# Optimization experiments

Measured on AMD Instinct MI355X. Metric: run time of the kernel, lower is better.

Reference implementation:

```python
import jax, jax.numpy as jnp
import numpy as np

SECURE_MIN = 1e-5
EPS = 1e-20
N_ITER = 10

def _l1_normalize(t, axis):
    # F.normalize(p=1): t / max(||t||_1, eps); t is nonnegative here so |t| = t
    n = jnp.sum(jnp.abs(t), axis=axis, keepdims=True)
    return t / jnp.maximum(n, EPS)

def setup_inputs() -> dict:
    key = jax.random.key(0)
    kx, kw = jax.random.split(key)
    B, F_in, F_out = 2048, 4096, 2048
    x = jax.random.uniform(kx, (B, F_in), dtype=jnp.float32)
    W = jax.random.uniform(kw, (F_out, F_in), dtype=jnp.float32)
    return {"x": x, "W": W}

def reference(x, W):
    B = x.shape[0]
    F_out = W.shape[0]
    # normalize_weights: clamp to secure min, L1-normalize each row (over input dim)
    Wn = _l1_normalize(jnp.clip(W, SECURE_MIN), axis=1)  # (F_out, F_in)
    # _prepare_input: L1 normalize over feature dim
    xn = _l1_normalize(x, axis=-1)  # (B, F_in)
    # _reset_h: uniform h over output units
    h0 = jnp.full((B, F_out), 1.0 / F_out, dtype=x.dtype)

    def step(h, _):
        # _reconstruct: h @ W -> input space
        recon = h @ Wn                                   # (B, F_in)
        recon = jnp.clip(recon, SECURE_MIN)              # _secure_tensor
        recon = _l1_normalize(recon, axis=-1)            # normalize_reconstruction
        update = (xn / recon) @ Wn.T                     # _forward, (B, F_out)
        h = h * update                                   # multiplicative NNMF update
        h = _l1_normalize(jnp.clip(h, SECURE_MIN), axis=-1)  # _process_h
        return h, None

    h, _ = jax.lax.scan(step, h0, None, length=N_ITER)
    return h
```

## Files before the change

### kernel.cpp

```cpp
#include <hip/hip_runtime.h>
#include <stdint.h>
#include <stddef.h>

#define B_DIM 2048
#define FIN   4096
#define FOUT  2048
#define NITER 10
#define SMIN  1e-5f

#define WSCALE 16384.0f
#define HSCALE 256.0f
#define OUTSCALE1 (1.0f / 4194304.0f)
#define RS_I8 56.0f

typedef float floatx16 __attribute__((ext_vector_type(16)));
typedef int   intx4    __attribute__((ext_vector_type(4)));
typedef int   intx8    __attribute__((ext_vector_type(8)));
typedef int   intx16   __attribute__((ext_vector_type(16)));

__device__ inline unsigned short f2bf(float f) {
    unsigned int u = __float_as_uint(f);
    u += 0x7fffu + ((u >> 16) & 1u);
    return (unsigned short)(u >> 16);
}
__device__ inline float bflo(unsigned int u) { return __uint_as_float(u << 16); }
__device__ inline float bfhi(unsigned int u) { return __uint_as_float(u & 0xffff0000u); }
__device__ inline unsigned int pack2(float a, float b) {
    return (unsigned int)f2bf(a) | ((unsigned int)f2bf(b) << 16);
}
__device__ inline unsigned short f2h(float f) {
    union { _Float16 h; unsigned short u; } c;
    c.h = (_Float16)f;
    return c.u;
}
__device__ inline float h2f(unsigned short u) {
    union { _Float16 h; unsigned short u; } c;
    c.u = u;
    return (float)c.h;
}

__device__ inline void async16(const void* g, void* l) {
    __builtin_amdgcn_global_load_lds(
        (const __attribute__((address_space(1))) void*)g,
        (__attribute__((address_space(3))) void*)l, 16, 0, 0);
}

__device__ inline float block_row_sum(float v) {
    #pragma unroll
    for (int o = 32; o > 0; o >>= 1) v += __shfl_down(v, o, 64);
    __shared__ float red[4];
    const int lane = threadIdx.x & 63, w = threadIdx.x >> 6;
    if (lane == 0) red[w] = v;
    __syncthreads();
    return red[0] + red[1] + red[2] + red[3];
}

__device__ inline void block_sum_max(float s, float m, float* os, float* om) {
    #pragma unroll
    for (int o = 32; o > 0; o >>= 1) {
        s += __shfl_down(s, o, 64);
        m = fmaxf(m, __shfl_down(m, o, 64));
    }
    __shared__ float rs[4], rm[4];
    const int lane = threadIdx.x & 63, w = threadIdx.x >> 6;
    if (lane == 0) { rs[w] = s; rm[w] = m; }
    __syncthreads();
    *os = (rs[0] + rs[1]) + (rs[2] + rs[3]);
    *om = fmaxf(fmaxf(rm[0], rm[1]), fmaxf(rm[2], rm[3]));
}

__global__ __launch_bounds__(256) void k_norm_w(const float* __restrict__ W,
                                                unsigned char* __restrict__ Wn8,
                                                unsigned char* __restrict__ WnI8,
                                                float* __restrict__ dq) {
    const int row = blockIdx.x;
    const float4* src = (const float4*)(W + (size_t)row * FIN);
    float4 vals[4];
    float s = 0.f, m = 0.f;
    #pragma unroll
    for (int i = 0; i < 4; ++i) {
        float4 v = src[i * 256 + threadIdx.x];
        v.x = fmaxf(v.x, SMIN); v.y = fmaxf(v.y, SMIN);
        v.z = fmaxf(v.z, SMIN); v.w = fmaxf(v.w, SMIN);
        vals[i] = v;
        s += (v.x + v.y) + (v.z + v.w);
        m = fmaxf(m, fmaxf(fmaxf(v.x, v.y), fmaxf(v.z, v.w)));
    }
    block_sum_max(s, m, &s, &m);
    s = fmaxf(s, 1e-20f);
    const float inv8 = WSCALE / s;
    const float qi = 126.f / m;
    if (threadIdx.x == 0) dq[row] = m / (126.f * RS_I8 * s);
    unsigned int* d8 = (unsigned int*)(Wn8 + (size_t)row * FIN);
    unsigned int* di = (unsigned int*)(WnI8 + (size_t)row * FIN);
    #pragma unroll
    for (int i = 0; i < 4; ++i) {
        float4 v = vals[i];
        unsigned int u = 0;
        u = (unsigned int)__builtin_amdgcn_cvt_pk_fp8_f32(v.x * inv8, v.y * inv8, (int)u, false);
        u = (unsigned int)__builtin_amdgcn_cvt_pk_fp8_f32(v.z * inv8, v.w * inv8, (int)u, true);
        d8[i * 256 + threadIdx.x] = u;
        const int b0 = (int)(v.x * qi + 0.5f);
        const int b1 = (int)(v.y * qi + 0.5f);
        const int b2 = (int)(v.z * qi + 0.5f);
        const int b3 = (int)(v.w * qi + 0.5f);
        di[i * 256 + threadIdx.x] =
            (unsigned int)b0 | ((unsigned int)b1 << 8) |
            ((unsigned int)b2 << 16) | ((unsigned int)b3 << 24);
    }
}

__global__ __launch_bounds__(256) void k_norm_x(const float* __restrict__ x,
                                                unsigned int* __restrict__ xnb) {
    const int row = blockIdx.x;
    const float4* src = (const float4*)(x + (size_t)row * FIN);
    float4 vals[4];
    float s = 0.f;
    #pragma unroll
    for (int j = 0; j < 2; ++j) {
        const int idx = j * 256 + threadIdx.x;
        float4 a = src[2 * idx], b = src[2 * idx + 1];
        vals[2 * j] = a; vals[2 * j + 1] = b;
        s += (fabsf(a.x) + fabsf(a.y)) + (fabsf(a.z) + fabsf(a.w));
        s += (fabsf(b.x) + fabsf(b.y)) + (fabsf(b.z) + fabsf(b.w));
    }
    s = block_row_sum(s);
    const float inv = 1.f / fmaxf(s, 1e-20f);
    uint4* dst = (uint4*)(xnb + (size_t)row * (FIN / 2));
    #pragma unroll
    for (int j = 0; j < 2; ++j) {
        float4 a = vals[2 * j], b = vals[2 * j + 1];
        uint4 o;
        o.x = pack2(a.x * inv, a.y * inv);
        o.y = pack2(a.z * inv, a.w * inv);
        o.z = pack2(b.x * inv, b.y * inv);
        o.w = pack2(b.z * inv, b.w * inv);
        dst[j * 256 + threadIdx.x] = o;
    }
}

__global__ __launch_bounds__(256) void k_transpose_fp8(const unsigned char* __restrict__ src,
                                                       unsigned char* __restrict__ dst) {
    __shared__ unsigned char tile[32][33];
    const int bi = blockIdx.x * 32, bo = blockIdx.y * 32;
    const int tx = threadIdx.x, ty = threadIdx.y;
    #pragma unroll
    for (int j = 0; j < 4; ++j)
        tile[ty + j * 8][tx] = src[(size_t)(bo + ty + j * 8) * FIN + bi + tx];
    __syncthreads();
    #pragma unroll
    for (int j = 0; j < 4; ++j)
        dst[(size_t)(bi + ty + j * 8) * FOUT + bo + tx] = tile[tx][ty + j * 8];
}

__global__ __launch_bounds__(256) void k_init_h(unsigned int* __restrict__ h16,
                                                unsigned int* __restrict__ h8u) {
    const int i = blockIdx.x * blockDim.x + threadIdx.x;
    uint2 v; v.x = 0x10001000u; v.y = 0x10001000u;
    ((uint2*)h16)[i] = v;
    h8u[i] = 0x20202020u;
}

__global__ __launch_bounds__(256) void k_gemm_fp8(const unsigned char* __restrict__ A,
                                                  const unsigned char* __restrict__ Bm,
                                                  unsigned short* __restrict__ C,
                                                  int N, int K) {
    __shared__ __align__(16) unsigned char As[2][128 * 128];
    __shared__ __align__(16) unsigned char Bs[2][128 * 128];
    const int tid  = threadIdx.x;
    const int wave = tid >> 6;
    const int lane = tid & 63;

    const int id = blockIdx.y * 32 + blockIdx.x;
    const int j8 = id & 7, s = id >> 3;
    const int bm = ((j8 >> 2) * 8 + (s >> 3)) * 128;
    const int bn = ((j8 & 3) * 8 + (s & 7)) * 128;

    const int wr = (wave >> 1) * 64;
    const int wc = (wave & 1) * 64;
    const int l31 = lane & 31;
    const int half = lane >> 5;

    floatx16 acc[2][2] = {};

    const int lr = lane >> 3;
    const int ks = ((lane & 7) ^ lr) * 16;
    const unsigned char* ga = A  + (size_t)(bm + wave * 32 + lr) * K + ks;
    const unsigned char* gb = Bm + (size_t)(bn + wave * 32 + lr) * K + ks;

    auto stage = [&](int k0, int buf) {
        #pragma unroll
        for (int j = 0; j < 4; ++j) {
            async16(ga + (size_t)j * 8 * K + k0, &As[buf][wave * 4096 + j * 1024]);
            async16(gb + (size_t)j * 8 * K + k0, &Bs[buf][wave * 4096 + j * 1024]);
        }
    };

    const int nt = K >> 7;
    stage(0, 0);
    int cur = 0;
    for (int t = 0; t < nt; ++t) {
        __syncthreads();
        if (t + 1 < nt) stage((t + 1) << 7, cur ^ 1);

        const int sw = l31 & 7;
        #pragma unroll
        for (int m = 0; m < 2; ++m) {
            const int c0 = ((4 * m + 2 * half) ^ sw) << 4;
            const int c1 = ((4 * m + 2 * half + 1) ^ sw) << 4;
            intx8 af[2], bf[2];
            #pragma unroll
            for (int tt = 0; tt < 2; ++tt) {
                const int ra = (wr + tt * 32 + l31) * 128;
                const int rb = (wc + tt * 32 + l31) * 128;
                intx4 a0 = *(const intx4*)&As[cur][ra + c0];
                intx4 a1 = *(const intx4*)&As[cur][ra + c1];
                intx4 b0 = *(const intx4*)&Bs[cur][rb + c0];
                intx4 b1 = *(const intx4*)&Bs[cur][rb + c1];
                af[tt] = (intx8){a0.x, a0.y, a0.z, a0.w, a1.x, a1.y, a1.z, a1.w};
                bf[tt] = (intx8){b0.x, b0.y, b0.z, b0.w, b1.x, b1.y, b1.z, b1.w};
            }
            #pragma unroll
            for (int mt = 0; mt < 2; ++mt)
                #pragma unroll
                for (int nt2 = 0; nt2 < 2; ++nt2)
                    acc[mt][nt2] = __builtin_amdgcn_mfma_scale_f32_32x32x64_f8f6f4(
                        af[mt], bf[nt2], acc[mt][nt2],
                        0, 0, 0, 0x7F7F7F7Fu, 0, 0x7F7F7F7Fu);
        }
        cur ^= 1;
    }

    const int row0 = 4 * half;
    #pragma unroll
    for (int mt = 0; mt < 2; ++mt) {
        #pragma unroll
        for (int nt2 = 0; nt2 < 2; ++nt2) {
            #pragma unroll
            for (int reg = 0; reg < 16; ++reg) {
                const int rr = bm + wr + mt * 32 + row0 + (reg & 3) + 8 * (reg >> 2);
                const int cc = bn + wc + nt2 * 32 + l31;
                C[(size_t)rr * N + cc] = f2bf(acc[mt][nt2][reg] * OUTSCALE1);
            }
        }
    }
}

__global__ __launch_bounds__(256) void k_gemm_i8(const unsigned char* __restrict__ A,
                                                 const unsigned char* __restrict__ Bm,
                                                 const float* __restrict__ dq,
                                                 unsigned short* __restrict__ C,
                                                 int N, int K, int Ksub) {
    __shared__ __align__(16) unsigned char As[2][128 * 128];
    __shared__ __align__(16) unsigned char Bs[2][128 * 128];
    const int tid  = threadIdx.x;
    const int wave = tid >> 6;
    const int lane = tid & 63;

    const int id = blockIdx.y * 16 + blockIdx.x;
    const int j8 = id & 7, s = id >> 3;
    const int bm = ((j8 >> 1) * 4 + (s >> 3)) * 128;
    const int bn = ((j8 & 1) * 8 + (s & 7)) * 128;

    const int kz = blockIdx.z * Ksub;
    const int wr = (wave >> 1) * 64;
    const int wc = (wave & 1) * 64;
    const int l31 = lane & 31;
    const int half = lane >> 5;

    intx16 acc[2][2] = {};

    const int lr = lane >> 3;
    const int ks = ((lane & 7) ^ lr) * 16;
    const unsigned char* ga = A  + (size_t)(bm + wave * 32 + lr) * K + ks;
    const unsigned char* gb = Bm + (size_t)(bn + wave * 32 + lr) * K + ks;

    auto stage = [&](int k0, int buf) {
        #pragma unroll
        for (int j = 0; j < 4; ++j) {
            async16(ga + (size_t)j * 8 * K + k0, &As[buf][wave * 4096 + j * 1024]);
            async16(gb + (size_t)j * 8 * K + k0, &Bs[buf][wave * 4096 + j * 1024]);
        }
    };

    const int nt = Ksub >> 7;
    stage(kz, 0);
    int cur = 0;
    for (int t = 0; t < nt; ++t) {
        __syncthreads();
        if (t + 1 < nt) stage(kz + ((t + 1) << 7), cur ^ 1);

        const int sw = l31 & 7;
        #pragma unroll
        for (int kk = 0; kk < 4; ++kk) {
            const int slot = ((2 * kk + half) ^ sw) << 4;
            intx4 af[2], bf[2];
            #pragma unroll
            for (int tt = 0; tt < 2; ++tt) {
                af[tt] = *(const intx4*)&As[cur][(wr + tt * 32 + l31) * 128 + slot];
                bf[tt] = *(const intx4*)&Bs[cur][(wc + tt * 32 + l31) * 128 + slot];
            }
            #pragma unroll
            for (int mt = 0; mt < 2; ++mt)
                #pragma unroll
                for (int nt2 = 0; nt2 < 2; ++nt2)
                    acc[mt][nt2] = __builtin_amdgcn_mfma_i32_32x32x32_i8(
                        af[mt], bf[nt2], acc[mt][nt2], 0, 0, 0);
        }
        cur ^= 1;
    }

    unsigned short* Cz = C + (size_t)blockIdx.z * B_DIM * N;
    const int row0 = 4 * half;
    const float d0 = dq[bn + wc + l31];
    const float d1 = dq[bn + wc + 32 + l31];
    #pragma unroll
    for (int mt = 0; mt < 2; ++mt) {
        #pragma unroll
        for (int nt2 = 0; nt2 < 2; ++nt2) {
            const float d = nt2 ? d1 : d0;
            #pragma unroll
            for (int reg = 0; reg < 16; ++reg) {
                const int rr = bm + wr + mt * 32 + row0 + (reg & 3) + 8 * (reg >> 2);
                const int cc = bn + wc + nt2 * 32 + l31;
                Cz[(size_t)rr * N + cc] = f2h((float)acc[mt][nt2][reg] * d);
            }
        }
    }
}

__global__ __launch_bounds__(256) void k_make_ratio(const unsigned short* __restrict__ rec,
                                                    const unsigned int* __restrict__ xnb,
                                                    unsigned char* __restrict__ ri8) {
    const int row = blockIdx.x;
    float v[16];
    float s = 0.f;
    #pragma unroll
    for (int g = 0; g < 2; ++g) {
        const int idx = g * 256 + threadIdx.x;
        uint4 u = ((const uint4*)(rec + (size_t)row * FIN))[idx];
        float* p = v + g * 8;
        p[0] = bflo(u.x); p[1] = bfhi(u.x); p[2] = bflo(u.y); p[3] = bfhi(u.y);
        p[4] = bflo(u.z); p[5] = bfhi(u.z); p[6] = bflo(u.w); p[7] = bfhi(u.w);
        #pragma unroll
        for (int e = 0; e < 8; ++e) { p[e] = fmaxf(p[e], SMIN); s += p[e]; }
    }
    s = block_row_sum(s);
    const float ss = s * RS_I8;
    #pragma unroll
    for (int g = 0; g < 2; ++g) {
        const int idx = g * 256 + threadIdx.x;
        uint4 xu = ((const uint4*)(xnb + (size_t)row * (FIN / 2)))[idx];
        float* p = v + g * 8;
        float r[8];
        r[0] = bflo(xu.x) * ss / p[0]; r[1] = bfhi(xu.x) * ss / p[1];
        r[2] = bflo(xu.y) * ss / p[2]; r[3] = bfhi(xu.y) * ss / p[3];
        r[4] = bflo(xu.z) * ss / p[4]; r[5] = bfhi(xu.z) * ss / p[5];
        r[6] = bflo(xu.w) * ss / p[6]; r[7] = bfhi(xu.w) * ss / p[7];
        unsigned int q[8];
        #pragma unroll
        for (int e = 0; e < 8; ++e)
            q[e] = (unsigned int)(int)(fminf(r[e], 127.0f) + 0.5f);
        uint2 o;
        o.x = q[0] | (q[1] << 8) | (q[2] << 16) | (q[3] << 24);
        o.y = q[4] | (q[5] << 8) | (q[6] << 16) | (q[7] << 24);
        ((uint2*)(ri8 + (size_t)row * FIN))[idx] = o;
    }
}

__global__ __launch_bounds__(256) void k_update_h(const unsigned short* __restrict__ hin,
                                                  const unsigned short* __restrict__ upd,
                                                  int nparts,
                                                  unsigned short* __restrict__ hout,
                                                  float* __restrict__ outf,
                                                  unsigned int* __restrict__ h8u) {
    const int row = blockIdx.x;
    float4 vals[2];
    float s = 0.f;
    #pragma unroll
    for (int i = 0; i < 2; ++i) {
        const int idx = i * 256 + threadIdx.x;
        uint2 hu = ((const uint2*)(hin + (size_t)row * FOUT))[idx];
        float4 hv;
        hv.x = h2f((unsigned short)(hu.x & 0xffffu));
        hv.y = h2f((unsigned short)(hu.x >> 16));
        hv.z = h2f((unsigned short)(hu.y & 0xffffu));
        hv.w = h2f((unsigned short)(hu.y >> 16));
        uint2 u = ((const uint2*)(upd + (size_t)row * FOUT))[idx];
        float4 uv;
        uv.x = h2f((unsigned short)(u.x & 0xffffu));
        uv.y = h2f((unsigned short)(u.x >> 16));
        uv.z = h2f((unsigned short)(u.y & 0xffffu));
        uv.w = h2f((unsigned short)(u.y >> 16));
        for (int z = 1; z < nparts; ++z) {
            uint2 q = ((const uint2*)(upd + (size_t)z * B_DIM * FOUT + (size_t)row * FOUT))[idx];
            uv.x += h2f((unsigned short)(q.x & 0xffffu));
            uv.y += h2f((unsigned short)(q.x >> 16));
            uv.z += h2f((unsigned short)(q.y & 0xffffu));
            uv.w += h2f((unsigned short)(q.y >> 16));
        }
        float4 v;
        v.x = fmaxf(hv.x * uv.x, SMIN);
        v.y = fmaxf(hv.y * uv.y, SMIN);
        v.z = fmaxf(hv.z * uv.z, SMIN);
        v.w = fmaxf(hv.w * uv.w, SMIN);
        vals[i] = v;
        s += (v.x + v.y) + (v.z + v.w);
    }
    s = block_row_sum(s);
    const float inv = 1.f / fmaxf(s, 1e-20f);
    unsigned int* bp = h8u + (size_t)row * (FOUT / 4);
    #pragma unroll
    for (int i = 0; i < 2; ++i) {
        const int idx = i * 256 + threadIdx.x;
        float4 v = vals[i];
        v.x *= inv; v.y *= inv; v.z *= inv; v.w *= inv;
        if (outf) {
            ((float4*)(outf + (size_t)row * FOUT))[idx] = v;
        } else {
            uint2 o;
            o.x = (unsigned int)f2h(v.x) | ((unsigned int)f2h(v.y) << 16);
            o.y = (unsigned int)f2h(v.z) | ((unsigned int)f2h(v.w) << 16);
            ((uint2*)(hout + (size_t)row * FOUT))[idx] = o;
        }
        unsigned int u = 0;
        u = (unsigned int)__builtin_amdgcn_cvt_pk_fp8_f32(v.x * HSCALE, v.y * HSCALE, (int)u, false);
        u = (unsigned int)__builtin_amdgcn_cvt_pk_fp8_f32(v.z * HSCALE, v.w * HSCALE, (int)u, true);
        bp[idx] = u;
    }
}

extern "C" void kernel_launch(void* const* d_in, const int* in_sizes, int n_in,
                              void* d_out, int out_size, void* d_ws, size_t ws_size,
                              hipStream_t stream) {
    const float* x = (const float*)d_in[0];
    const float* W = (const float*)d_in[1];
    float* out = (float*)d_out;

    const size_t UPD_PART = (size_t)B_DIM * FOUT * 2;
    const size_t FIXED    = 81000000;
    int S2 = 1;
    if (ws_size >= FIXED + 2 * UPD_PART + (1 << 20)) {
        S2 = 2;
    }

    char* ws = (char*)d_ws;
    size_t off = 0;
    auto alloc = [&](size_t bytes) {
        void* p = ws + off;
        off += (bytes + 255) & ~(size_t)255;
        return p;
    };
    unsigned char*  WnT8 = (unsigned char*)alloc((size_t)FIN * FOUT);
    unsigned char*  WnI8 = (unsigned char*)alloc((size_t)FOUT * FIN);
    float*          dq   = (float*)alloc((size_t)FOUT * 4);
    unsigned int*   h8u  = (unsigned int*)alloc((size_t)B_DIM * FOUT);
    unsigned char*  ri8  = (unsigned char*)alloc((size_t)B_DIM * FIN);
    unsigned int*   xnb  = (unsigned int*)alloc((size_t)B_DIM * FIN * 2);
    unsigned short* h16  = (unsigned short*)alloc((size_t)B_DIM * FOUT * 2);
    unsigned short* rec  = (unsigned short*)alloc((size_t)B_DIM * FIN * 2);
    unsigned short* upd  = (unsigned short*)alloc(UPD_PART * S2);
    unsigned char* Wn8 = (unsigned char*)rec;
    (void)in_sizes; (void)n_in; (void)out_size;

    k_norm_w<<<FOUT, 256, 0, stream>>>(W, Wn8, WnI8, dq);
    k_transpose_fp8<<<dim3(FIN / 32, FOUT / 32), dim3(32, 8), 0, stream>>>(Wn8, WnT8);
    k_norm_x<<<B_DIM, 256, 0, stream>>>(x, xnb);
    k_init_h<<<(B_DIM * FOUT) / (256 * 4), 256, 0, stream>>>((unsigned int*)h16, h8u);

    for (int it = 0; it < NITER; ++it) {
        k_gemm_fp8<<<dim3(FIN / 128, B_DIM / 128, 1), 256, 0, stream>>>(
            (const unsigned char*)h8u, WnT8, rec, FIN, FOUT);
        k_make_ratio<<<B_DIM, 256, 0, stream>>>(rec, xnb, ri8);
        k_gemm_i8<<<dim3(FOUT / 128, B_DIM / 128, S2), 256, 0, stream>>>(
            ri8, WnI8, dq, upd, FOUT, FIN, FIN / S2);
        k_update_h<<<B_DIM, 256, 0, stream>>>(
            h16, upd, S2, h16, (it == NITER - 1) ? out : nullptr, h8u);
    }
}
```

Measured before the change: 725.0 us.

## Widen GEMM block tiles to 128x256 with 64x128 per-wave tiles

Both the fp8 and int8 GEMM kernels now compute a 128x256 output tile per block instead of 128x128. Each wave holds a 2x4 grid of 32x32 accumulators, and the cooperative global-to-LDS staging, swizzle, grid size and block-id remapping are rewritten to match. The aim is to raise arithmetic intensity per LDS and global byte and to halve the number of blocks. The cost is double the accumulator registers and more LDS (96KB double-buffered), which lowers occupancy. With fewer blocks on a 256-CU part, the number of blocks per wave of work may also become uneven.

After: 841.0 us. 16.0% more time.

```diff
diff --git a/kernel.cpp b/kernel.cpp
--- a/kernel.cpp
+++ b/kernel.cpp
@@ -166,34 +166,35 @@
                                                   unsigned short* __restrict__ C,
                                                   int N, int K) {
     __shared__ __align__(16) unsigned char As[2][128 * 128];
-    __shared__ __align__(16) unsigned char Bs[2][128 * 128];
+    __shared__ __align__(16) unsigned char Bs[2][256 * 128];
     const int tid  = threadIdx.x;
     const int wave = tid >> 6;
     const int lane = tid & 63;
 
-    const int id = blockIdx.y * 32 + blockIdx.x;
+    const int id = blockIdx.y * 16 + blockIdx.x;
     const int j8 = id & 7, s = id >> 3;
-    const int bm = ((j8 >> 2) * 8 + (s >> 3)) * 128;
-    const int bn = ((j8 & 3) * 8 + (s & 7)) * 128;
+    const int bm = ((j8 >> 2) * 8 + (s >> 2)) * 128;
+    const int bn = ((j8 & 3) * 4 + (s & 3)) * 256;
 
     const int wr = (wave >> 1) * 64;
-    const int wc = (wave & 1) * 64;
+    const int wc = (wave & 1) * 128;
     const int l31 = lane & 31;
     const int half = lane >> 5;
 
-    floatx16 acc[2][2] = {};
-
-    const int lr = lane >> 3;
-    const int ks = ((lane & 7) ^ lr) * 16;
-    const unsigned char* ga = A  + (size_t)(bm + wave * 32 + lr) * K + ks;
-    const unsigned char* gb = Bm + (size_t)(bn + wave * 32 + lr) * K + ks;
+    floatx16 acc[2][4] = {};
+
+    const int r0 = tid >> 3;
+    const int ksw = (((tid & 7) ^ (r0 & 7)) << 4);
+    const unsigned char* ga = A  + (size_t)(bm + r0) * K + ksw;
+    const unsigned char* gb = Bm + (size_t)(bn + r0) * K + ksw;
 
     auto stage = [&](int k0, int buf) {
         #pragma unroll
-        for (int j = 0; j < 4; ++j) {
-            async16(ga + (size_t)j * 8 * K + k0, &As[buf][wave * 4096 + j * 1024]);
-            async16(gb + (size_t)j * 8 * K + k0, &Bs[buf][wave * 4096 + j * 1024]);
-        }
+        for (int j = 0; j < 4; ++j)
+            async16(ga + (size_t)(j * 32) * K + k0, &As[buf][j * 4096 + tid * 16]);
+        #pragma unroll
+        for (int j = 0; j < 8; ++j)
+            async16(gb + (size_t)(j * 32) * K + k0, &Bs[buf][j * 4096 + tid * 16]);
     };
 
     const int nt = K >> 7;
@@ -205,25 +206,28 @@
 
         const int sw = l31 & 7;
         #pragma unroll
-        for (int m = 0; m < 2; ++m) {
-            const int c0 = ((4 * m + 2 * half) ^ sw) << 4;
-            const int c1 = ((4 * m + 2 * half + 1) ^ sw) << 4;
-            intx8 af[2], bf[2];
-            #pragma unroll
-            for (int tt = 0; tt < 2; ++tt) {
-                const int ra = (wr + tt * 32 + l31) * 128;
-                const int rb = (wc + tt * 32 + l31) * 128;
+        for (int g = 0; g < 2; ++g) {
+            const int c0 = ((4 * g + 2 * half) ^ sw) << 4;
+            const int c1 = ((4 * g + 2 * half + 1) ^ sw) << 4;
+            intx8 af[2], bf[4];
+            #pragma unroll
+            for (int mt = 0; mt < 2; ++mt) {
+                const int ra = (wr + mt * 32 + l31) * 128;
                 intx4 a0 = *(const intx4*)&As[cur][ra + c0];
                 intx4 a1 = *(const intx4*)&As[cur][ra + c1];
+                af[mt] = (intx8){a0.x, a0.y, a0.z, a0.w, a1.x, a1.y, a1.z, a1.w};
+            }
+            #pragma unroll
+            for (int nt2 = 0; nt2 < 4; ++nt2) {
+                const int rb = (wc + nt2 * 32 + l31) * 128;
                 intx4 b0 = *(const intx4*)&Bs[cur][rb + c0];
                 intx4 b1 = *(const intx4*)&Bs[cur][rb + c1];
-                af[tt] = (intx8){a0.x, a0.y, a0.z, a0.w, a1.x, a1.y, a1.z, a1.w};
-                bf[tt] = (intx8){b0.x, b0.y, b0.z, b0.w, b1.x, b1.y, b1.z, b1.w};
+                bf[nt2] = (intx8){b0.x, b0.y, b0.z, b0.w, b1.x, b1.y, b1.z, b1.w};
             }
             #pragma unroll
             for (int mt = 0; mt < 2; ++mt)
                 #pragma unroll
-                for (int nt2 = 0; nt2 < 2; ++nt2)
+                for (int nt2 = 0; nt2 < 4; ++nt2)
                     acc[mt][nt2] = __builtin_amdgcn_mfma_scale_f32_32x32x64_f8f6f4(
                         af[mt], bf[nt2], acc[mt][nt2],
                         0, 0, 0, 0x7F7F7F7Fu, 0, 0x7F7F7F7Fu);
@@ -235,7 +239,7 @@
     #pragma unroll
     for (int mt = 0; mt < 2; ++mt) {
         #pragma unroll
-        for (int nt2 = 0; nt2 < 2; ++nt2) {
+        for (int nt2 = 0; nt2 < 4; ++nt2) {
             #pragma unroll
             for (int reg = 0; reg < 16; ++reg) {
                 const int rr = bm + wr + mt * 32 + row0 + (reg & 3) + 8 * (reg >> 2);
@@ -252,35 +256,36 @@
                                                  unsigned short* __restrict__ C,
                                                  int N, int K, int Ksub) {
     __shared__ __align__(16) unsigned char As[2][128 * 128];
-    __shared__ __align__(16) unsigned char Bs[2][128 * 128];
+    __shared__ __align__(16) unsigned char Bs[2][256 * 128];
     const int tid  = threadIdx.x;
     const int wave = tid >> 6;
     const int lane = tid & 63;
 
-    const int id = blockIdx.y * 16 + blockIdx.x;
+    const int id = blockIdx.y * 8 + blockIdx.x;
     const int j8 = id & 7, s = id >> 3;
-    const int bm = ((j8 >> 1) * 4 + (s >> 3)) * 128;
-    const int bn = ((j8 & 1) * 8 + (s & 7)) * 128;
+    const int bm = ((j8 >> 1) * 4 + (s >> 2)) * 128;
+    const int bn = ((j8 & 1) * 4 + (s & 3)) * 256;
 
     const int kz = blockIdx.z * Ksub;
     const int wr = (wave >> 1) * 64;
-    const int wc = (wave & 1) * 64;
+    const int wc = (wave & 1) * 128;
     const int l31 = lane & 31;
     const int half = lane >> 5;
 
-    intx16 acc[2][2] = {};
-
-    const int lr = lane >> 3;
-    const int ks = ((lane & 7) ^ lr) * 16;
-    const unsigned char* ga = A  + (size_t)(bm + wave * 32 + lr) * K + ks;
-    const unsigned char* gb = Bm + (size_t)(bn + wave * 32 + lr) * K + ks;
+    intx16 acc[2][4] = {};
+
+    const int r0 = tid >> 3;
+    const int ksw = (((tid & 7) ^ (r0 & 7)) << 4);
+    const unsigned char* ga = A  + (size_t)(bm + r0) * K + ksw;
+    const unsigned char* gb = Bm + (size_t)(bn + r0) * K + ksw;
 
     auto stage = [&](int k0, int buf) {
         #pragma unroll
-        for (int j = 0; j < 4; ++j) {
-            async16(ga + (size_t)j * 8 * K + k0, &As[buf][wave * 4096 + j * 1024]);
-            async16(gb + (size_t)j * 8 * K + k0, &Bs[buf][wave * 4096 + j * 1024]);
-        }
+        for (int j = 0; j < 4; ++j)
+            async16(ga + (size_t)(j * 32) * K + k0, &As[buf][j * 4096 + tid * 16]);
+        #pragma unroll
+        for (int j = 0; j < 8; ++j)
+            async16(gb + (size_t)(j * 32) * K + k0, &Bs[buf][j * 4096 + tid * 16]);
     };
 
     const int nt = Ksub >> 7;
@@ -294,16 +299,17 @@
         #pragma unroll
         for (int kk = 0; kk < 4; ++kk) {
             const int slot = ((2 * kk + half) ^ sw) << 4;
-            intx4 af[2], bf[2];
-            #pragma unroll
-            for (int tt = 0; tt < 2; ++tt) {
-                af[tt] = *(const intx4*)&As[cur][(wr + tt * 32 + l31) * 128 + slot];
-                bf[tt] = *(const intx4*)&Bs[cur][(wc + tt * 32 + l31) * 128 + slot];
-            }
+            intx4 af[2], bf[4];
+            #pragma unroll
+            for (int mt = 0; mt < 2; ++mt)
+                af[mt] = *(const intx4*)&As[cur][(wr + mt * 32 + l31) * 128 + slot];
+            #pragma unroll
+            for (int nt2 = 0; nt2 < 4; ++nt2)
+                bf[nt2] = *(const intx4*)&Bs[cur][(wc + nt2 * 32 + l31) * 128 + slot];
             #pragma unroll
             for (int mt = 0; mt < 2; ++mt)
                 #pragma unroll
-                for (int nt2 = 0; nt2 < 2; ++nt2)
+                for (int nt2 = 0; nt2 < 4; ++nt2)
                     acc[mt][nt2] = __builtin_amdgcn_mfma_i32_32x32x32_i8(
                         af[mt], bf[nt2], acc[mt][nt2], 0, 0, 0);
         }
@@ -312,18 +318,19 @@
 
     unsigned short* Cz = C + (size_t)blockIdx.z * B_DIM * N;
     const int row0 = 4 * half;
-    const float d0 = dq[bn + wc + l31];
-    const float d1 = dq[bn + wc + 32 + l31];
+    float d[4];
+    #pragma unroll
+    for (int nt2 = 0; nt2 < 4; ++nt2)
+        d[nt2] = dq[bn + wc + nt2 * 32 + l31];
     #pragma unroll
     for (int mt = 0; mt < 2; ++mt) {
         #pragma unroll
-        for (int nt2 = 0; nt2 < 2; ++nt2) {
-            const float d = nt2 ? d1 : d0;
+        for (int nt2 = 0; nt2 < 4; ++nt2) {
             #pragma unroll
             for (int reg = 0; reg < 16; ++reg) {
                 const int rr = bm + wr + mt * 32 + row0 + (reg & 3) + 8 * (reg >> 2);
                 const int cc = bn + wc + nt2 * 32 + l31;
-                Cz[(size_t)rr * N + cc] = f2h((float)acc[mt][nt2][reg] * d);
+                Cz[(size_t)rr * N + cc] = f2h((float)acc[mt][nt2][reg] * d[nt2]);
             }
         }
     }
@@ -469,10 +476,10 @@
     k_init_h<<<(B_DIM * FOUT) / (256 * 4), 256, 0, stream>>>((unsigned int*)h16, h8u);
 
     for (int it = 0; it < NITER; ++it) {
-        k_gemm_fp8<<<dim3(FIN / 128, B_DIM / 128, 1), 256, 0, stream>>>(
+        k_gemm_fp8<<<dim3(FIN / 256, B_DIM / 128), 256, 0, stream>>>(
             (const unsigned char*)h8u, WnT8, rec, FIN, FOUT);
         k_make_ratio<<<B_DIM, 256, 0, stream>>>(rec, xnb, ri8);
-        k_gemm_i8<<<dim3(FOUT / 128, B_DIM / 128, S2), 256, 0, stream>>>(
+        k_gemm_i8<<<dim3(FOUT / 256, B_DIM / 128, S2), 256, 0, stream>>>(
             ri8, WnI8, dq, upd, FOUT, FIN, FIN / S2);
         k_update_h<<<B_DIM, 256, 0, stream>>>(
             h16, upd, S2, h16, (it == NITER - 1) ? out : nullptr, h8u);
```
